# Optimization experiments

Hardware: AMD Instinct MI355X
Metric: run time of the kernel (lower is better)

Reference implementation:

```python
import jax, jax.numpy as jnp
import numpy as np

N = 8000      # nodes (spatial spots)
E = 40000     # directed edges (kNN graph, avg degree 5)
DIN = 1024    # input_dim
H = 3         # heads
C = 1024      # hidden_dim per head
NCLS = 460    # n_classes
NCEN = 100    # centroid count (pass-through only)
NEG_SLOPE = 0.2


def setup_inputs() -> dict:
    key = jax.random.key(0)
    ks = jax.random.split(key, 12)
    s_in = 1.0 / np.sqrt(DIN)   # glorot-ish scale for 1024 fan-in
    s_h = 1.0 / np.sqrt(C)
    return {
        'x': jax.random.normal(ks[0], (N, DIN), jnp.float32),
        'edge_index': jax.random.randint(ks[1], (E, 2), 0, N),  # [E,2] (src,dst)
        'Wl': jax.random.normal(ks[2], (DIN, H * C), jnp.float32) * s_in,
        'bl': jnp.zeros((H * C,), jnp.float32),
        'Wr': jax.random.normal(ks[3], (DIN, H * C), jnp.float32) * s_in,
        'br': jnp.zeros((H * C,), jnp.float32),
        'att': jax.random.normal(ks[4], (H, C), jnp.float32) * s_h,
        'bias': jnp.zeros((C,), jnp.float32),
        'Wf': jax.random.normal(ks[5], (C, NCLS), jnp.float32) * s_h,
        'bf': jnp.zeros((NCLS,), jnp.float32),
        'exps': jax.random.uniform(ks[6], (N, NCLS), jnp.float32),
        'exps_c': jax.random.uniform(ks[7], (NCEN, NCLS), jnp.float32),
    }


def reference(x, edge_index, Wl, bl, Wr, br, att, bias, Wf, bf, exps, exps_c):
    n = x.shape[0]
    h_, c_ = att.shape
    # PyG GATv2Conv default add_self_loops=True
    loops = jnp.arange(n)
    src = jnp.concatenate([edge_index[:, 0], loops])
    dst = jnp.concatenate([edge_index[:, 1], loops])
    # lin_l / lin_r projections -> [N,H,C]
    xl = (x @ Wl + bl).reshape(n, h_, c_)
    xr = (x @ Wr + br).reshape(n, h_, c_)
    # GATv2 edge scores: a^T LeakyReLU(x_l[src] + x_r[dst])  -> [Etot,H]
    s = jax.nn.leaky_relu(xl[src] + xr[dst], NEG_SLOPE)
    e = jnp.einsum('ehc,hc->eh', s, att)
    # segment softmax over incoming edges per dst node (PyG softmax: +1e-16)
    m = jax.lax.stop_gradient(jax.ops.segment_max(e, dst, num_segments=n))
    a = jnp.exp(e - m[dst])
    denom = jax.ops.segment_sum(a, dst, num_segments=n)
    alpha = a / (denom[dst] + 1e-16)
    # weighted scatter-add of source messages
    out = jax.ops.segment_sum(alpha[:, :, None] * xl[src], dst, num_segments=n)
    # concat=False -> mean over heads, then conv bias
    out = out.mean(axis=1) + bias
    # fc + row softmax
    h = jax.nn.softmax(out @ Wf + bf, axis=-1)
    return h
```

## Files before the change

### kernel.cpp

```cpp
#include <hip/hip_runtime.h>

#define NNODES 8000
#define MPAD   8192
#define NEDGES 40000
#define ETOT   (NEDGES + NNODES)
#define DIN    1024
#define NH     3
#define CH     1024
#define HC     (NH * CH)
#define NTOT   (2 * HC)
#define NCLS   460
#define NCLS_P 512
#define NEG    0.2f

typedef _Float16 h8 __attribute__((ext_vector_type(8)));
typedef _Float16 h4v __attribute__((ext_vector_type(4)));
typedef float    f4 __attribute__((ext_vector_type(4)));

#define GLOAD16(g, l) \
    __builtin_amdgcn_global_load_lds((const __attribute__((address_space(1))) void*)(g), \
                                     (__attribute__((address_space(3))) void*)(l), 16, 0, 0)

__global__ __launch_bounds__(256)
void fp16_pad_convert(const float* __restrict__ in, _Float16* __restrict__ out,
                      int rows_in, int rows_out, int cols)
{
    size_t i4 = (size_t)blockIdx.x * 256 + threadIdx.x;
    size_t tot = ((size_t)rows_out * cols) >> 2;
    if (i4 >= tot) return;
    size_t e = i4 << 2;
    int row = (int)(e / cols);
    float vx = 0.f, vy = 0.f, vz = 0.f, vw = 0.f;
    if (row < rows_in) {
        float4 v = *(const float4*)(in + e);
        vx = v.x; vy = v.y; vz = v.z; vw = v.w;
    }
    h4v o = { (_Float16)vx, (_Float16)vy, (_Float16)vz, (_Float16)vw };
    *(h4v*)(out + e) = o;
}

__global__ __launch_bounds__(256)
void transpose_to_fp16(const float* __restrict__ W, _Float16* __restrict__ Wt,
                       int K, int Ncols, int rowOff)
{
    __shared__ float tile[32][33];
    int n0 = blockIdx.x * 32, k0 = blockIdx.y * 32;
    int tx = threadIdx.x, ty = threadIdx.y;
    #pragma unroll
    for (int i = 0; i < 4; ++i) {
        int k = k0 + ty + i * 8;
        int n = n0 + tx;
        tile[ty + i * 8][tx] = (n < Ncols) ? W[(size_t)k * Ncols + n] : 0.f;
    }
    __syncthreads();
    #pragma unroll
    for (int i = 0; i < 4; ++i) {
        int n = n0 + ty + i * 8;
        int k = k0 + tx;
        Wt[(size_t)(rowOff + n) * K + k] = (_Float16)tile[tx][ty + i * 8];
    }
}

__global__ __launch_bounds__(256)
void bias_pack(const float* __restrict__ bl, const float* __restrict__ br,
               const float* __restrict__ bf, const float* __restrict__ att,
               float* __restrict__ b1, float* __restrict__ b2, _Float16* __restrict__ atth)
{
    int i = blockIdx.x * 256 + threadIdx.x;
    if (i < HC) { b1[i] = bl[i]; b1[HC + i] = br[i]; atth[i] = (_Float16)att[i]; }
    if (i < NCLS_P) b2[i] = (i < NCLS) ? bf[i] : 0.f;
}

__global__ __launch_bounds__(256)
void csr_count(const int* __restrict__ ei, int* __restrict__ cnt)
{
    int e = blockIdx.x * 256 + threadIdx.x;
    if (e >= ETOT) return;
    int dst = (e < NEDGES) ? ei[2 * e + 1] : (e - NEDGES);
    atomicAdd(&cnt[dst], 1);
}

__global__ __launch_bounds__(1024)
void csr_scan(const int* __restrict__ cnt, int* __restrict__ rofs)
{
    __shared__ int s[1024];
    int t = threadIdx.x;
    int base = t * 8;
    int local[8];
    int sum = 0;
    #pragma unroll
    for (int i = 0; i < 8; ++i) {
        local[i] = sum;
        sum += (base + i < NNODES) ? cnt[base + i] : 0;
    }
    s[t] = sum;
    __syncthreads();
    for (int off = 1; off < 1024; off <<= 1) {
        int v = (t >= off) ? s[t - off] : 0;
        __syncthreads();
        if (t >= off) s[t] += v;
        __syncthreads();
    }
    int pre = (t > 0) ? s[t - 1] : 0;
    #pragma unroll
    for (int i = 0; i < 8; ++i)
        if (base + i < NNODES) rofs[base + i] = pre + local[i];
}

__global__ __launch_bounds__(256)
void csr_fill(const int* __restrict__ ei, const int* __restrict__ rofs,
              int* __restrict__ cursor, int* __restrict__ csr_src)
{
    int e = blockIdx.x * 256 + threadIdx.x;
    if (e >= ETOT) return;
    int src, dst;
    if (e < NEDGES) { src = ei[2 * e]; dst = ei[2 * e + 1]; }
    else            { src = dst = e - NEDGES; }
    int pos = rofs[dst] + atomicAdd(&cursor[dst], 1);
    csr_src[pos] = src;
}

__global__ __launch_bounds__(512, 2)
void gemm256_f16(const _Float16* __restrict__ A, const _Float16* __restrict__ Bt,
                 const float* __restrict__ biasN, _Float16* __restrict__ C16,
                 int N, int K)
{
    __shared__ __align__(16) _Float16 lds[65536];

    int nwg = gridDim.x;
    int orig = blockIdx.x;
    int cpx = nwg >> 3;
    int wg = (orig & 7) * cpx + (orig >> 3);
    int nbx = N >> 8;
    int bm = wg / nbx, bn = wg - bm * nbx;
    int m0 = bm << 8, n0 = bn << 8;

    const int t = threadIdx.x;
    const int lane = t & 63;
    const int w = t >> 6;
    const int wm = w >> 2;
    const int wn = w & 3;

    const int sRow = lane >> 3;
    const int sCol = (lane & 7) << 3;
    const int seg0 = w << 1;

    const int l15 = lane & 15;
    const int kl8 = (lane >> 4) << 3;

    f4 acc[8][4];
    f4 zero = { 0.f, 0.f, 0.f, 0.f };
    #pragma unroll
    for (int i = 0; i < 8; ++i)
        #pragma unroll
        for (int j = 0; j < 4; ++j) acc[i][j] = zero;

    auto STAGE_A = [&](int kt, int h, int b) {
        const _Float16* src = A + (size_t)(m0 + h * 128 + seg0 * 8 + sRow) * K + kt * 64 + sCol;
        int dst = b * 32768 + h * 8192 + seg0 * 512;
        GLOAD16(src, &lds[dst]);
        GLOAD16(src + (size_t)8 * K, &lds[dst + 512]);
    };
    auto STAGE_B = [&](int kt, int h, int b) {
        const _Float16* src = Bt + (size_t)(n0 + h * 128 + seg0 * 8 + sRow) * K + kt * 64 + sCol;
        int dst = b * 32768 + 16384 + h * 8192 + seg0 * 512;
        GLOAD16(src, &lds[dst]);
        GLOAD16(src + (size_t)8 * K, &lds[dst + 512]);
    };

    h8 bfr[4][2];
    const int aBase = wm * 128 + l15;
    const int bBase = wn * 64 + l15;

#define DS_A(fi, ks2, q, b) (*(const h8*)&lds[(b)*32768 + (aBase + (q)*32 + (fi)*16)*64 + (ks2)*32 + kl8])
#define DS_B(nf, ks2, b)    (*(const h8*)&lds[(b)*32768 + 16384 + (bBase + (nf)*16)*64 + (ks2)*32 + kl8])

#define PHASE(b, q, STAGE_STMT, VMEND)                                                            \
    {                                                                                             \
        h8 a00 = DS_A(0, 0, q, b), a01 = DS_A(0, 1, q, b);                                        \
        h8 a10 = DS_A(1, 0, q, b), a11 = DS_A(1, 1, q, b);                                        \
        if ((q) == 0) {                                                                           \
            _Pragma("unroll")                                                                     \
            for (int nf = 0; nf < 4; ++nf) {                                                      \
                bfr[nf][0] = DS_B(nf, 0, b);                                                      \
                bfr[nf][1] = DS_B(nf, 1, b);                                                      \
            }                                                                                     \
        }                                                                                         \
        STAGE_STMT;                                                                               \
        __builtin_amdgcn_s_barrier();                                                             \
        asm volatile("s_waitcnt lgkmcnt(0)" ::: "memory");                                        \
        __builtin_amdgcn_sched_barrier(0);                                                        \
        __builtin_amdgcn_s_setprio(1);                                                            \
        _Pragma("unroll")                                                                         \
        for (int nf = 0; nf < 4; ++nf) {                                                          \
            acc[(q)*2+0][nf] = __builtin_amdgcn_mfma_f32_16x16x32_f16(a00, bfr[nf][0], acc[(q)*2+0][nf], 0, 0, 0); \
            acc[(q)*2+0][nf] = __builtin_amdgcn_mfma_f32_16x16x32_f16(a01, bfr[nf][1], acc[(q)*2+0][nf], 0, 0, 0); \
            acc[(q)*2+1][nf] = __builtin_amdgcn_mfma_f32_16x16x32_f16(a10, bfr[nf][0], acc[(q)*2+1][nf], 0, 0, 0); \
            acc[(q)*2+1][nf] = __builtin_amdgcn_mfma_f32_16x16x32_f16(a11, bfr[nf][1], acc[(q)*2+1][nf], 0, 0, 0); \
        }                                                                                         \
        __builtin_amdgcn_s_setprio(0);                                                            \
        if (VMEND) asm volatile("s_waitcnt vmcnt(4)" ::: "memory");                               \
        __builtin_amdgcn_s_barrier();                                                             \
    }

    STAGE_A(0, 0, 0); STAGE_A(0, 1, 0);
    STAGE_B(0, 0, 0); STAGE_B(0, 1, 0);
    STAGE_B(1, 0, 1); STAGE_B(1, 1, 1);
    asm volatile("s_waitcnt vmcnt(4)" ::: "memory");
    __builtin_amdgcn_s_barrier();

    const int NKT = K >> 6;
    for (int kt = 0; kt < NKT; kt += 2) {
        PHASE(0, 0, STAGE_A(kt + 1, 0, 1), false);
        PHASE(0, 1, STAGE_A(kt + 1, 1, 1), false);
        PHASE(0, 2, STAGE_B(kt + 2, 0, 0), false);
        PHASE(0, 3, STAGE_B(kt + 2, 1, 0), true);
        PHASE(1, 0, STAGE_A(kt + 2, 0, 0), false);
        PHASE(1, 1, STAGE_A(kt + 2, 1, 0), false);
        PHASE(1, 2, STAGE_B(kt + 3, 0, 1), false);
        PHASE(1, 3, STAGE_B(kt + 3, 1, 1), true);
    }

#undef PHASE
#undef DS_A
#undef DS_B

    #pragma unroll
    for (int mf = 0; mf < 8; ++mf) {
        int row0 = m0 + wm * 128 + mf * 16 + ((lane >> 4) << 2);
        #pragma unroll
        for (int nf = 0; nf < 4; ++nf) {
            int col = n0 + wn * 64 + nf * 16 + l15;
            float bb = biasN[col];
            #pragma unroll
            for (int rg = 0; rg < 4; ++rg)
                C16[(size_t)(row0 + rg) * N + col] = (_Float16)(acc[mf][nf][rg] + bb);
        }
    }
}

__global__ __launch_bounds__(256, 4)
void gemm_f16(const _Float16* __restrict__ A, const _Float16* __restrict__ Bt,
              const float* __restrict__ biasN,
              float* __restrict__ C32, _Float16* __restrict__ C16,
              int N, int K)
{
    __shared__ __align__(16) _Float16 sA[128 * 32];
    __shared__ __align__(16) _Float16 sB[128 * 32];

    int nwg = gridDim.x;
    int orig = blockIdx.x;
    int q = nwg >> 3, r = nwg & 7;
    int xcd = orig & 7, idx = orig >> 3;
    int wg = (xcd < r ? xcd * (q + 1) : r * (q + 1) + (xcd - r) * q) + idx;
    int nbx = N >> 7;
    int bm = wg / nbx, bn = wg - bm * nbx;
    int m0 = bm << 7, n0 = bn << 7;

    const int t = threadIdx.x;
    const int lane = t & 63, w = t >> 6;
    const int wr = (w >> 1) << 6, wc = (w & 1) << 6;

    f4 acc[4][4];
    f4 zero = { 0.f, 0.f, 0.f, 0.f };
    #pragma unroll
    for (int i = 0; i < 4; ++i)
        #pragma unroll
        for (int j = 0; j < 4; ++j) acc[i][j] = zero;

    const int lr = lane >> 2, lk = lane & 3;
    const _Float16* gA = A  + (size_t)(m0 + w * 16 + lr) * K + lk * 8;
    const _Float16* gB = Bt + (size_t)(n0 + w * 16 + lr) * K + lk * 8;
    _Float16* lA0 = &sA[w * 512];
    _Float16* lA1 = &sA[2048 + w * 512];
    _Float16* lB0 = &sB[w * 512];
    _Float16* lB1 = &sB[2048 + w * 512];
    const size_t seg = (size_t)64 * K;

    const int nk = K >> 5;
    for (int s = 0; s < nk; ++s) {
        const int ko = s << 5;
        GLOAD16(gA + ko,       lA0);
        GLOAD16(gA + seg + ko, lA1);
        GLOAD16(gB + ko,       lB0);
        GLOAD16(gB + seg + ko, lB1);
        __syncthreads();
        const int ks = lane >> 4;
        h8 bh[4];
        #pragma unroll
        for (int nj = 0; nj < 4; ++nj)
            bh[nj] = *(const h8*)&sB[(wc + nj * 16 + (lane & 15)) * 32 + ks * 8];
        #pragma unroll
        for (int mi = 0; mi < 4; ++mi) {
            h8 ah = *(const h8*)&sA[(wr + mi * 16 + (lane & 15)) * 32 + ks * 8];
            #pragma unroll
            for (int nj = 0; nj < 4; ++nj)
                acc[mi][nj] = __builtin_amdgcn_mfma_f32_16x16x32_f16(ah, bh[nj], acc[mi][nj], 0, 0, 0);
        }
        __syncthreads();
    }

    #pragma unroll
    for (int mi = 0; mi < 4; ++mi) {
        #pragma unroll
        for (int nj = 0; nj < 4; ++nj) {
            int col  = n0 + wc + nj * 16 + (lane & 15);
            int rowb = m0 + wr + mi * 16 + ((lane >> 4) << 2);
            float b = biasN[col];
            #pragma unroll
            for (int rg = 0; rg < 4; ++rg) {
                float v = acc[mi][nj][rg] + b;
                size_t off = (size_t)(rowb + rg) * N + col;
                if (C32) C32[off] = v;
                else     C16[off] = (_Float16)v;
            }
        }
    }
}

__global__ __launch_bounds__(256)
void edge_fused(const _Float16* __restrict__ xlr, const int* __restrict__ rofs,
                const int* __restrict__ cnt, const int* __restrict__ csr_src,
                const _Float16* __restrict__ atth, const float* __restrict__ bias,
                _Float16* __restrict__ o2h)
{
    const int wid = threadIdx.x >> 6;
    const int dst = (blockIdx.x << 2) + wid;
    const int l   = threadIdx.x & 63;
    const int cb0 = l << 3, cb1 = 512 + (l << 3);

    h8 xr[3][2], at[3][2];
    #pragma unroll
    for (int h = 0; h < 3; ++h) {
        const _Float16* pr = xlr + (size_t)dst * NTOT + HC + h * CH;
        xr[h][0] = *(const h8*)(pr + cb0);
        xr[h][1] = *(const h8*)(pr + cb1);
        at[h][0] = *(const h8*)(atth + h * CH + cb0);
        at[h][1] = *(const h8*)(atth + h * CH + cb1);
    }

    const int beg = rofs[dst];
    const int num = cnt[dst];

    float m[3] = { -3.4e38f, -3.4e38f, -3.4e38f };
    float d[3] = { 0.f, 0.f, 0.f };
    float acc[3][2][8] = {};

    for (int i = 0; i < num; ++i) {
        int src = csr_src[beg + i];
        const _Float16* ps = xlr + (size_t)src * NTOT;
        h8 xv[3][2];
        #pragma unroll
        for (int h = 0; h < 3; ++h) {
            xv[h][0] = *(const h8*)(ps + h * CH + cb0);
            xv[h][1] = *(const h8*)(ps + h * CH + cb1);
        }
        #pragma unroll
        for (int h = 0; h < 3; ++h) {
            float s = 0.f;
            #pragma unroll
            for (int b = 0; b < 2; ++b)
                #pragma unroll
                for (int j = 0; j < 8; ++j) {
                    float z = (float)xv[h][b][j] + (float)xr[h][b][j];
                    z = z > 0.f ? z : NEG * z;
                    s = fmaf((float)at[h][b][j], z, s);
                }
            #pragma unroll
            for (int off = 32; off > 0; off >>= 1) s += __shfl_xor(s, off);
            float nm = fmaxf(m[h], s);
            float rs = __expf(m[h] - nm);
            float wt = __expf(s - nm);
            d[h] = d[h] * rs + wt;
            #pragma unroll
            for (int b = 0; b < 2; ++b)
                #pragma unroll
                for (int j = 0; j < 8; ++j)
                    acc[h][b][j] = fmaf(wt, (float)xv[h][b][j], acc[h][b][j] * rs);
            m[h] = nm;
        }
    }

    float inv0 = 1.f / (d[0] + 1e-16f) * (1.f / 3.f);
    float inv1 = 1.f / (d[1] + 1e-16f) * (1.f / 3.f);
    float inv2 = 1.f / (d[2] + 1e-16f) * (1.f / 3.f);
    #pragma unroll
    for (int b = 0; b < 2; ++b) {
        int c = b ? cb1 : cb0;
        h8 o;
        #pragma unroll
        for (int j = 0; j < 8; ++j) {
            float v = acc[0][b][j] * inv0 + acc[1][b][j] * inv1 + acc[2][b][j] * inv2
                    + bias[c + j];
            o[j] = (_Float16)v;
        }
        *(h8*)(o2h + (size_t)dst * CH + c) = o;
    }
}

__global__ __launch_bounds__(64)
void row_softmax(const float* __restrict__ logits, float* __restrict__ out)
{
    const int r = blockIdx.x;
    const int lane = threadIdx.x;
    const float* row = logits + (size_t)r * NCLS_P;
    float v[8];
    float mx = -3.4e38f;
    #pragma unroll
    for (int i = 0; i < 8; ++i) {
        int c = lane + i * 64;
        v[i] = (c < NCLS) ? row[c] : -3.4e38f;
        mx = fmaxf(mx, v[i]);
    }
    #pragma unroll
    for (int off = 32; off > 0; off >>= 1) mx = fmaxf(mx, __shfl_xor(mx, off));
    float s = 0.f;
    #pragma unroll
    for (int i = 0; i < 8; ++i) {
        int c = lane + i * 64;
        float ev = (c < NCLS) ? expf(v[i] - mx) : 0.f;
        v[i] = ev;
        s += ev;
    }
    #pragma unroll
    for (int off = 32; off > 0; off >>= 1) s += __shfl_xor(s, off);
    float inv = 1.f / s;
    #pragma unroll
    for (int i = 0; i < 8; ++i) {
        int c = lane + i * 64;
        if (c < NCLS) out[(size_t)r * NCLS + c] = v[i] * inv;
    }
}

extern "C" void kernel_launch(void* const* d_in, const int* in_sizes, int n_in,
                              void* d_out, int out_size, void* d_ws, size_t ws_size,
                              hipStream_t stream)
{
    (void)in_sizes; (void)n_in; (void)out_size; (void)ws_size;

    const float* x    = (const float*)d_in[0];
    const int*   ei   = (const int*)  d_in[1];
    const float* Wl   = (const float*)d_in[2];
    const float* bl   = (const float*)d_in[3];
    const float* Wr   = (const float*)d_in[4];
    const float* br   = (const float*)d_in[5];
    const float* att  = (const float*)d_in[6];
    const float* bias = (const float*)d_in[7];
    const float* Wf   = (const float*)d_in[8];
    const float* bf   = (const float*)d_in[9];

    char* base = (char*)d_ws;
    _Float16* xh      = (_Float16*)(base);
    _Float16* BtW     = (_Float16*)(base + 16777216);
    _Float16* Wft     = (_Float16*)(base + 29360128);
    float*    biasC1  = (float*)   (base + 30408704);
    float*    biasC2  = (float*)   (base + 30433280);
    _Float16* atth    = (_Float16*)(base + 30435328);
    int*      cnt     = (int*)     (base + 30441472);
    int*      cursor  = (int*)     (base + 30473472);
    int*      rofs    = (int*)     (base + 30505472);
    int*      csr_src = (int*)     (base + 30537472);
    _Float16* o2h     = (_Float16*)(base + 30729472);
    float*    logits  = (float*)   (base + 47506688);
    _Float16* xlr     = (_Float16*)(base + 64283904);

    hipMemsetAsync(cnt, 0, 64000, stream);
    hipMemsetAsync(o2h + (size_t)NNODES * CH, 0, (size_t)(MPAD - NNODES) * CH * 2, stream);

    fp16_pad_convert<<<(MPAD * DIN / 4 + 255) / 256, 256, 0, stream>>>(
        x, xh, NNODES, MPAD, DIN);

    transpose_to_fp16<<<dim3(HC / 32, DIN / 32), dim3(32, 8), 0, stream>>>(Wl, BtW, DIN, HC, 0);
    transpose_to_fp16<<<dim3(HC / 32, DIN / 32), dim3(32, 8), 0, stream>>>(Wr, BtW, DIN, HC, HC);
    transpose_to_fp16<<<dim3(NCLS_P / 32, DIN / 32), dim3(32, 8), 0, stream>>>(Wf, Wft, DIN, NCLS, 0);

    bias_pack<<<(HC + 255) / 256, 256, 0, stream>>>(bl, br, bf, att, biasC1, biasC2, atth);

    csr_count<<<(ETOT + 255) / 256, 256, 0, stream>>>(ei, cnt);
    csr_scan<<<1, 1024, 0, stream>>>(cnt, rofs);
    csr_fill<<<(ETOT + 255) / 256, 256, 0, stream>>>(ei, rofs, cursor, csr_src);

    gemm256_f16<<<(MPAD / 256) * (NTOT / 256), 512, 0, stream>>>(
        xh, BtW, biasC1, xlr, NTOT, DIN);

    edge_fused<<<NNODES / 4, 256, 0, stream>>>(xlr, rofs, cnt, csr_src, atth, bias, o2h);

    gemm_f16<<<(NCLS_P / 128) * (MPAD / 128), 256, 0, stream>>>(
        o2h, Wft, biasC2, logits, nullptr, NCLS_P, DIN);

    row_softmax<<<NNODES, 64, 0, stream>>>(logits, (float*)d_out);
}
```

Before: 422.8 us.

## Swizzle GEMM LDS layout and split edge kernel heads across wavefronts

```diff
diff --git a/kernel.cpp b/kernel.cpp
--- a/kernel.cpp
+++ b/kernel.cpp
@@ -141,12 +141,11 @@
     const int wm = w >> 2;
     const int wn = w & 3;
 
-    const int sRow = lane >> 3;
-    const int sCol = (lane & 7) << 3;
-    const int seg0 = w << 1;
+    const int sRow   = lane >> 3;
+    const int sColSw = (((lane & 7) ^ sRow) << 3);
+    const int seg0   = w << 1;
 
     const int l15 = lane & 15;
-    const int kl8 = (lane >> 4) << 3;
 
     f4 acc[8][4];
     f4 zero = { 0.f, 0.f, 0.f, 0.f };
@@ -156,13 +155,13 @@
         for (int j = 0; j < 4; ++j) acc[i][j] = zero;
 
     auto STAGE_A = [&](int kt, int h, int b) {
-        const _Float16* src = A + (size_t)(m0 + h * 128 + seg0 * 8 + sRow) * K + kt * 64 + sCol;
+        const _Float16* src = A + (size_t)(m0 + h * 128 + seg0 * 8 + sRow) * K + kt * 64 + sColSw;
         int dst = b * 32768 + h * 8192 + seg0 * 512;
         GLOAD16(src, &lds[dst]);
         GLOAD16(src + (size_t)8 * K, &lds[dst + 512]);
     };
     auto STAGE_B = [&](int kt, int h, int b) {
-        const _Float16* src = Bt + (size_t)(n0 + h * 128 + seg0 * 8 + sRow) * K + kt * 64 + sCol;
+        const _Float16* src = Bt + (size_t)(n0 + h * 128 + seg0 * 8 + sRow) * K + kt * 64 + sColSw;
         int dst = b * 32768 + 16384 + h * 8192 + seg0 * 512;
         GLOAD16(src, &lds[dst]);
         GLOAD16(src + (size_t)8 * K, &lds[dst + 512]);
@@ -172,8 +171,9 @@
     const int aBase = wm * 128 + l15;
     const int bBase = wn * 64 + l15;
 
-#define DS_A(fi, ks2, q, b) (*(const h8*)&lds[(b)*32768 + (aBase + (q)*32 + (fi)*16)*64 + (ks2)*32 + kl8])
-#define DS_B(nf, ks2, b)    (*(const h8*)&lds[(b)*32768 + 16384 + (bBase + (nf)*16)*64 + (ks2)*32 + kl8])
+#define SWC(ks2) (((((ks2) * 4 + (lane >> 4)) ^ (l15 & 7)) << 3))
+#define DS_A(fi, ks2, q, b) (*(const h8*)&lds[(b)*32768 + (aBase + (q)*32 + (fi)*16)*64 + SWC(ks2)])
+#define DS_B(nf, ks2, b)    (*(const h8*)&lds[(b)*32768 + 16384 + (bBase + (nf)*16)*64 + SWC(ks2)])
 
 #define PHASE(b, q, STAGE_STMT, VMEND)                                                            \
     {                                                                                             \
@@ -224,6 +224,7 @@
 #undef PHASE
 #undef DS_A
 #undef DS_B
+#undef SWC
 
     #pragma unroll
     for (int mf = 0; mf < 8; ++mf) {
@@ -318,80 +319,82 @@
     }
 }
 
-__global__ __launch_bounds__(256)
-void edge_fused(const _Float16* __restrict__ xlr, const int* __restrict__ rofs,
-                const int* __restrict__ cnt, const int* __restrict__ csr_src,
-                const _Float16* __restrict__ atth, const float* __restrict__ bias,
-                _Float16* __restrict__ o2h)
-{
-    const int wid = threadIdx.x >> 6;
-    const int dst = (blockIdx.x << 2) + wid;
+__global__ __launch_bounds__(192)
+void edge_fused3(const _Float16* __restrict__ xlr, const int* __restrict__ rofs,
+                 const int* __restrict__ cnt, const int* __restrict__ csr_src,
+                 const _Float16* __restrict__ atth, const float* __restrict__ bias,
+                 _Float16* __restrict__ o2h)
+{
+    __shared__ float comb[3 * CH];
+
+    const int dst = blockIdx.x;
+    const int h   = threadIdx.x >> 6;
     const int l   = threadIdx.x & 63;
     const int cb0 = l << 3, cb1 = 512 + (l << 3);
 
-    h8 xr[3][2], at[3][2];
-    #pragma unroll
-    for (int h = 0; h < 3; ++h) {
-        const _Float16* pr = xlr + (size_t)dst * NTOT + HC + h * CH;
-        xr[h][0] = *(const h8*)(pr + cb0);
-        xr[h][1] = *(const h8*)(pr + cb1);
-        at[h][0] = *(const h8*)(atth + h * CH + cb0);
-        at[h][1] = *(const h8*)(atth + h * CH + cb1);
-    }
+    const _Float16* pr = xlr + (size_t)dst * NTOT + HC + h * CH;
+    h8 xr0 = *(const h8*)(pr + cb0);
+    h8 xr1 = *(const h8*)(pr + cb1);
+    h8 at0 = *(const h8*)(atth + h * CH + cb0);
+    h8 at1 = *(const h8*)(atth + h * CH + cb1);
 
     const int beg = rofs[dst];
     const int num = cnt[dst];
 
-    float m[3] = { -3.4e38f, -3.4e38f, -3.4e38f };
-    float d[3] = { 0.f, 0.f, 0.f };
-    float acc[3][2][8] = {};
+    float m = -3.4e38f, d = 0.f;
+    float a0[8] = {}, a1[8] = {};
+
+    int src0 = csr_src[beg];
+    const _Float16* p0 = xlr + (size_t)src0 * NTOT + h * CH;
+    h8 nx0 = *(const h8*)(p0 + cb0);
+    h8 nx1 = *(const h8*)(p0 + cb1);
 
     for (int i = 0; i < num; ++i) {
-        int src = csr_src[beg + i];
-        const _Float16* ps = xlr + (size_t)src * NTOT;
-        h8 xv[3][2];
-        #pragma unroll
-        for (int h = 0; h < 3; ++h) {
-            xv[h][0] = *(const h8*)(ps + h * CH + cb0);
-            xv[h][1] = *(const h8*)(ps + h * CH + cb1);
-        }
-        #pragma unroll
-        for (int h = 0; h < 3; ++h) {
-            float s = 0.f;
-            #pragma unroll
-            for (int b = 0; b < 2; ++b)
-                #pragma unroll
-                for (int j = 0; j < 8; ++j) {
-                    float z = (float)xv[h][b][j] + (float)xr[h][b][j];
-                    z = z > 0.f ? z : NEG * z;
-                    s = fmaf((float)at[h][b][j], z, s);
-                }
-            #pragma unroll
-            for (int off = 32; off > 0; off >>= 1) s += __shfl_xor(s, off);
-            float nm = fmaxf(m[h], s);
-            float rs = __expf(m[h] - nm);
-            float wt = __expf(s - nm);
-            d[h] = d[h] * rs + wt;
-            #pragma unroll
-            for (int b = 0; b < 2; ++b)
-                #pragma unroll
-                for (int j = 0; j < 8; ++j)
-                    acc[h][b][j] = fmaf(wt, (float)xv[h][b][j], acc[h][b][j] * rs);
-            m[h] = nm;
-        }
-    }
-
-    float inv0 = 1.f / (d[0] + 1e-16f) * (1.f / 3.f);
-    float inv1 = 1.f / (d[1] + 1e-16f) * (1.f / 3.f);
-    float inv2 = 1.f / (d[2] + 1e-16f) * (1.f / 3.f);
-    #pragma unroll
-    for (int b = 0; b < 2; ++b) {
-        int c = b ? cb1 : cb0;
+        h8 xv0 = nx0, xv1 = nx1;
+        if (i + 1 < num) {
+            int s2 = csr_src[beg + i + 1];
+            const _Float16* p2 = xlr + (size_t)s2 * NTOT + h * CH;
+            nx0 = *(const h8*)(p2 + cb0);
+            nx1 = *(const h8*)(p2 + cb1);
+        }
+        float s = 0.f;
+        #pragma unroll
+        for (int j = 0; j < 8; ++j) {
+            float z0 = (float)xv0[j] + (float)xr0[j];
+            z0 = z0 > 0.f ? z0 : NEG * z0;
+            s = fmaf((float)at0[j], z0, s);
+            float z1 = (float)xv1[j] + (float)xr1[j];
+            z1 = z1 > 0.f ? z1 : NEG * z1;
+            s = fmaf((float)at1[j], z1, s);
+        }
+        #pragma unroll
+        for (int off = 32; off > 0; off >>= 1) s += __shfl_xor(s, off);
+        float nm = fmaxf(m, s);
+        float rs = __expf(m - nm);
+        float wt = __expf(s - nm);
+        d = d * rs + wt;
+        #pragma unroll
+        for (int j = 0; j < 8; ++j) {
+            a0[j] = fmaf(wt, (float)xv0[j], a0[j] * rs);
+            a1[j] = fmaf(wt, (float)xv1[j], a1[j] * rs);
+        }
+        m = nm;
+    }
+
+    float inv = 1.f / (d + 1e-16f) * (1.f / 3.f);
+    #pragma unroll
+    for (int j = 0; j < 8; ++j) {
+        comb[h * CH + cb0 + j] = a0[j] * inv;
+        comb[h * CH + cb1 + j] = a1[j] * inv;
+    }
+    __syncthreads();
+
+    if (threadIdx.x < 128) {
+        int c = threadIdx.x << 3;
         h8 o;
         #pragma unroll
         for (int j = 0; j < 8; ++j) {
-            float v = acc[0][b][j] * inv0 + acc[1][b][j] * inv1 + acc[2][b][j] * inv2
-                    + bias[c + j];
+            float v = comb[c + j] + comb[CH + c + j] + comb[2 * CH + c + j] + bias[c + j];
             o[j] = (_Float16)v;
         }
         *(h8*)(o2h + (size_t)dst * CH + c) = o;
@@ -483,7 +486,7 @@
     gemm256_f16<<<(MPAD / 256) * (NTOT / 256), 512, 0, stream>>>(
         xh, BtW, biasC1, xlr, NTOT, DIN);
 
-    edge_fused<<<NNODES / 4, 256, 0, stream>>>(xlr, rofs, cnt, csr_src, atth, bias, o2h);
+    edge_fused3<<<NNODES, 192, 0, stream>>>(xlr, rofs, cnt, csr_src, atth, bias, o2h);
 
     gemm_f16<<<(NCLS_P / 128) * (MPAD / 128), 256, 0, stream>>>(
         o2h, Wft, biasC2, logits, nullptr, NCLS_P, DIN);
```

Measured after the change: 351.3 us. 16.9% less time.
